# Optimization experiments

Hardware: AMD Instinct MI355X
Metric: run time of the kernel (lower is better)

Reference implementation:

```python
import jax, jax.numpy as jnp
import numpy as np

B, S, H, NH, I = 8, 1024, 1024, 16, 4096
HD = H // NH
EPS = 1e-6
NEG = -1e9


def _glorot(key, shape):
    lim = np.sqrt(6.0 / (shape[0] + shape[1]))
    return jax.random.uniform(key, shape, jnp.float32, -lim, lim)


def setup_inputs() -> dict:
    key = jax.random.key(0)
    ks = jax.random.split(key, 8)
    return {
        "inputs": jax.random.normal(ks[0], (B, S, H), jnp.float32),
        "inputs_mask": jnp.zeros((B, S), jnp.float32),  # 1.0 marks padding
        "attn_qkvw": _glorot(ks[1], (H, 3 * H)),
        "attn_qkvb": jnp.zeros((3 * H,), jnp.float32),
        "attn_ow": _glorot(ks[2], (H, H)),
        "attn_ob": jnp.zeros((H,), jnp.float32),
        "attn_nw": jnp.ones((H,), jnp.float32),
        "attn_nb": jnp.zeros((H,), jnp.float32),
        "inter_w": _glorot(ks[3], (H, I)),
        "inter_b": jnp.zeros((I,), jnp.float32),
        "output_w": _glorot(ks[4], (I, H)),
        "output_b": jnp.zeros((H,), jnp.float32),
        "ffn_nw": jnp.ones((H,), jnp.float32),
        "ffn_nb": jnp.zeros((H,), jnp.float32),
    }


def _layer_norm(x, g, b):
    m = jnp.mean(x, axis=-1, keepdims=True)
    v = jnp.mean(jnp.square(x - m), axis=-1, keepdims=True)
    return (x - m) * jax.lax.rsqrt(v + EPS) * g + b


def reference(inputs, inputs_mask, attn_qkvw, attn_qkvb, attn_ow, attn_ob,
              attn_nw, attn_nb, inter_w, inter_b, output_w, output_b,
              ffn_nw, ffn_nb):
    # ---- self-attention block (pre-LN) ----
    res = inputs
    x = _layer_norm(inputs, attn_nw, attn_nb)
    qkv = x @ attn_qkvw + attn_qkvb                      # [B,S,3H]
    q, k, v = jnp.split(qkv, 3, axis=-1)
    q = q.reshape(B, S, NH, HD)
    k = k.reshape(B, S, NH, HD)
    v = v.reshape(B, S, NH, HD)
    scale = 1.0 / np.sqrt(HD)
    scores = jnp.einsum("bqhd,bkhd->bhqk", q, k) * scale
    scores = scores + inputs_mask[:, None, None, :] * NEG
    probs = jax.nn.softmax(scores, axis=-1)
    ctx = jnp.einsum("bhqk,bkhd->bqhd", probs, v).reshape(B, S, H)
    attn_out = ctx @ attn_ow + attn_ob
    x = res + attn_out
    # ---- FFN block (pre-LN, ReLU) ----
    res2 = x
    y = _layer_norm(x, ffn_nw, ffn_nb)
    h = jax.nn.relu(y @ inter_w + inter_b)
    return res2 + h @ output_w + output_b
```

## Files before the change

kernel.cpp:

```cpp
#include <hip/hip_runtime.h>
#include <cstdint>
#include <cstddef>

typedef _Float16 f16;
typedef _Float16 half8 __attribute__((ext_vector_type(8)));
typedef _Float16 half4v __attribute__((ext_vector_type(4)));
typedef float floatx4 __attribute__((ext_vector_type(4)));
typedef float floatx16 __attribute__((ext_vector_type(16)));

__device__ __forceinline__ floatx4 mfma16(half8 a, half8 b, floatx4 c) {
    return __builtin_amdgcn_mfma_f32_16x16x32_f16(a, b, c, 0, 0, 0);
}
__device__ __forceinline__ floatx16 mfma32(half8 a, half8 b, floatx16 c) {
    return __builtin_amdgcn_mfma_f32_32x32x16_f16(a, b, c, 0, 0, 0);
}

__device__ __forceinline__ void async16(const f16* g, f16* l) {
    __builtin_amdgcn_global_load_lds(
        (const __attribute__((address_space(1))) unsigned int*)(uintptr_t)g,
        (__attribute__((address_space(3))) unsigned int*)(uintptr_t)l,
        16, 0, 0);
}

__global__ __launch_bounds__(256)
void ln_f16_kernel(const float* __restrict__ x, const float* __restrict__ g,
                   const float* __restrict__ be, f16* __restrict__ y)
{
    int row = blockIdx.x, t = threadIdx.x;
    const float* xr = x + (size_t)row * 1024;
    float4 v = *(const float4*)(xr + t * 4);
    float s1 = v.x + v.y + v.z + v.w;
    float s2 = v.x * v.x + v.y * v.y + v.z * v.z + v.w * v.w;
    #pragma unroll
    for (int off = 32; off >= 1; off >>= 1) {
        s1 += __shfl_xor(s1, off);
        s2 += __shfl_xor(s2, off);
    }
    __shared__ float r1[4], r2[4];
    if ((t & 63) == 0) { r1[t >> 6] = s1; r2[t >> 6] = s2; }
    __syncthreads();
    s1 = r1[0] + r1[1] + r1[2] + r1[3];
    s2 = r2[0] + r2[1] + r2[2] + r2[3];
    float mean = s1 * 0.0009765625f;
    float var  = s2 * 0.0009765625f - mean * mean;
    float rs = rsqrtf(var + 1e-6f);
    float4 gv = *(const float4*)(g + t * 4);
    float4 bv = *(const float4*)(be + t * 4);
    half4v o;
    o[0] = (f16)((v.x - mean) * rs * gv.x + bv.x);
    o[1] = (f16)((v.y - mean) * rs * gv.y + bv.y);
    o[2] = (f16)((v.z - mean) * rs * gv.z + bv.z);
    o[3] = (f16)((v.w - mean) * rs * gv.w + bv.w);
    *(half4v*)(y + (size_t)row * 1024 + t * 4) = o;
}

__global__ __launch_bounds__(256)
void transpose_f16_kernel(const float* __restrict__ W, f16* __restrict__ WT,
                          int R, int C)
{
    __shared__ float tile[32][33];
    int tx = threadIdx.x & 31, ty0 = threadIdx.x >> 5;
    int r0 = blockIdx.y * 32, c0 = blockIdx.x * 32;
    #pragma unroll
    for (int i = 0; i < 4; ++i)
        tile[ty0 + i * 8][tx] = W[(size_t)(r0 + ty0 + i * 8) * C + c0 + tx];
    __syncthreads();
    #pragma unroll
    for (int i = 0; i < 4; ++i)
        WT[(size_t)(c0 + ty0 + i * 8) * R + r0 + tx] = (f16)tile[tx][ty0 + i * 8];
}

__global__ __launch_bounds__(256, 2)
void gemm_kernel(const f16* __restrict__ A, const f16* __restrict__ BT,
                 const float* __restrict__ bias, const float* __restrict__ res,
                 float* __restrict__ Cf32, int M, int N, int K)
{
    __shared__ __align__(16) f16 As[2][128 * 64];
    __shared__ __align__(16) f16 Bs[2][128 * 64];
    int m0 = blockIdx.x * 128, n0 = blockIdx.y * 128;
    int t = threadIdx.x, lane = t & 63, wave = t >> 6;
    int quad = lane >> 4, l16 = lane & 15;
    int wm = (wave & 1) * 64, wn = (wave >> 1) * 64;
    int sw = l16 & 7;
    floatx4 acc[4][4] = {};

    const f16* gA[4]; const f16* gB[4]; int oS[4];
    #pragma unroll
    for (int c = 0; c < 4; ++c) {
        int s = c * 256 + t;
        int row = s >> 3, lg = (s & 7) ^ (row & 7);
        gA[c] = A  + (size_t)(m0 + row) * K + lg * 8;
        gB[c] = BT + (size_t)(n0 + row) * K + lg * 8;
        oS[c] = (c * 256 + (t & ~63)) * 8;
    }

    #pragma unroll
    for (int c = 0; c < 4; ++c) {
        async16(gA[c], As[0] + oS[c]);
        async16(gB[c], Bs[0] + oS[c]);
    }
    __syncthreads();

    int buf = 0;
    for (int k0 = 0; k0 < K; k0 += 64) {
        int kn = k0 + 64;
        if (kn < K) {
            #pragma unroll
            for (int c = 0; c < 4; ++c) {
                async16(gA[c] + kn, As[buf ^ 1] + oS[c]);
                async16(gB[c] + kn, Bs[buf ^ 1] + oS[c]);
            }
        }
        #pragma unroll
        for (int ks = 0; ks < 2; ++ks) {
            int ca = (ks * 4 + quad) ^ sw;
            half8 a[4], b[4];
            #pragma unroll
            for (int i = 0; i < 4; ++i) {
                a[i] = *(const half8*)(As[buf] + (wm + i * 16 + l16) * 64 + ca * 8);
                b[i] = *(const half8*)(Bs[buf] + (wn + i * 16 + l16) * 64 + ca * 8);
            }
            #pragma unroll
            for (int i = 0; i < 4; ++i)
                #pragma unroll
                for (int j = 0; j < 4; ++j)
                    acc[i][j] = mfma16(a[i], b[j], acc[i][j]);
        }
        __syncthreads();
        buf ^= 1;
    }

    #pragma unroll
    for (int j = 0; j < 4; ++j) {
        int col = n0 + wn + j * 16 + l16;
        float bv = bias[col];
        #pragma unroll
        for (int i = 0; i < 4; ++i) {
            int rowb = m0 + wm + i * 16 + quad * 4;
            #pragma unroll
            for (int r = 0; r < 4; ++r) {
                float v = acc[i][j][r] + bv;
                size_t idx = (size_t)(rowb + r) * N + col;
                Cf32[idx] = v + res[idx];
            }
        }
    }
}

template<int MODE>
__global__ __launch_bounds__(256, 2)
void gemm_big_kernel(const f16* __restrict__ A, const f16* __restrict__ BT,
                     const float* __restrict__ bias, f16* __restrict__ Cf16,
                     f16* __restrict__ qb, f16* __restrict__ kb, f16* __restrict__ vb,
                     int M, int N, int K)
{
    __shared__ __align__(16) f16 As[256 * 64];
    __shared__ __align__(16) f16 Bs[128 * 64];
    int m0 = blockIdx.x * 256, n0 = blockIdx.y * 128;
    int t = threadIdx.x, lane = t & 63, wave = t >> 6;
    int l32 = lane & 31, kg = lane >> 5;
    int swz = l32 & 7;
    floatx16 acc[2][4];
    #pragma unroll
    for (int mi = 0; mi < 2; ++mi)
        #pragma unroll
        for (int jn = 0; jn < 4; ++jn)
            #pragma unroll
            for (int r = 0; r < 16; ++r) acc[mi][jn][r] = 0.f;

    for (int k0 = 0; k0 < K; k0 += 64) {
        __syncthreads();
        #pragma unroll
        for (int c = 0; c < 8; ++c) {
            int s = c * 256 + t;
            int row = s >> 3, phys = s & 7;
            int lg = phys ^ (row & 7);
            async16(A + (size_t)(m0 + row) * K + k0 + lg * 8,
                    As + (size_t)(c * 256 + (t & ~63)) * 8);
        }
        #pragma unroll
        for (int c = 0; c < 4; ++c) {
            int s = c * 256 + t;
            int row = s >> 3, phys = s & 7;
            int lg = phys ^ (row & 7);
            async16(BT + (size_t)(n0 + row) * K + k0 + lg * 8,
                    Bs + (size_t)(c * 256 + (t & ~63)) * 8);
        }
        __syncthreads();
        #pragma unroll
        for (int ss = 0; ss < 4; ++ss) {
            int ca = (ss * 2 + kg) ^ swz;
            half8 a[2], b[4];
            #pragma unroll
            for (int mi = 0; mi < 2; ++mi)
                a[mi] = *(const half8*)(As + (wave * 64 + mi * 32 + l32) * 64 + ca * 8);
            #pragma unroll
            for (int jn = 0; jn < 4; ++jn)
                b[jn] = *(const half8*)(Bs + (jn * 32 + l32) * 64 + ca * 8);
            #pragma unroll
            for (int mi = 0; mi < 2; ++mi)
                #pragma unroll
                for (int jn = 0; jn < 4; ++jn)
                    acc[mi][jn] = mfma32(a[mi], b[jn], acc[mi][jn]);
        }
    }

    #pragma unroll
    for (int mi = 0; mi < 2; ++mi) {
        int mbase = m0 + wave * 64 + mi * 32 + 4 * kg;
        #pragma unroll
        for (int jn = 0; jn < 4; ++jn) {
            int col = n0 + jn * 32 + l32;
            float bv = bias[col];
            if (MODE == 1) {
                #pragma unroll
                for (int reg = 0; reg < 16; ++reg) {
                    int row = mbase + (reg & 3) + 8 * (reg >> 2);
                    Cf16[(size_t)row * N + col] = (f16)fmaxf(acc[mi][jn][reg] + bv, 0.f);
                }
            } else {
                int part = col >> 10;
                int h = (col >> 6) & 15;
                int d = col & 63;
                if (part == 2) {
                    #pragma unroll
                    for (int rb = 0; rb < 4; ++rb) {
                        int m = mbase + 8 * rb;
                        int bb = m >> 10, s = m & 1023;
                        size_t bh = (size_t)bb * 16 + h;
                        half4v pv;
                        #pragma unroll
                        for (int r = 0; r < 4; ++r) pv[r] = (f16)(acc[mi][jn][rb * 4 + r] + bv);
                        *(half4v*)(vb + (bh * 64 + d) * 1024 + s) = pv;
                    }
                } else {
                    f16* dst0 = part == 0 ? qb : kb;
                    #pragma unroll
                    for (int reg = 0; reg < 16; ++reg) {
                        int m = mbase + (reg & 3) + 8 * (reg >> 2);
                        int bb = m >> 10, s = m & 1023;
                        size_t bh = (size_t)bb * 16 + h;
                        dst0[(bh * 1024 + s) * 64 + d] = (f16)(acc[mi][jn][reg] + bv);
                    }
                }
            }
        }
    }
}

__global__ __launch_bounds__(256)
void attn_kernel(const f16* __restrict__ qb, const f16* __restrict__ kb,
                 const f16* __restrict__ vb, const float* __restrict__ mask,
                 f16* __restrict__ ctx)
{
    const int S = 1024;
    int qt = blockIdx.x, h = blockIdx.y, b = blockIdx.z;
    size_t bh = (size_t)b * 16 + h;
    int t = threadIdx.x, lane = t & 63, wv = t >> 6;
    int quad = lane >> 4, l16 = lane & 15;
    int sw = l16 & 7;

    __shared__ __align__(16) f16 Ks[64 * 64];
    __shared__ __align__(16) f16 Vs[64 * 64];
    __shared__ __align__(16) f16 Ps[4][16 * 40];

    int q0 = qt * 64 + wv * 16;
    const f16* qrow = qb + (bh * 1024 + q0 + l16) * 64;
    half8 aq0 = *(const half8*)(qrow + quad * 8);
    half8 aq1 = *(const half8*)(qrow + 32 + quad * 8);

    floatx4 o[4] = {};
    float lsum[4] = {0.f, 0.f, 0.f, 0.f};
    const float scale = 0.125f;
    const float* mrow = mask + b * S;

    for (int kc = 0; kc < S; kc += 64) {
        __syncthreads();
        #pragma unroll
        for (int c = 0; c < 2; ++c) {
            int s = c * 256 + t;
            int row = s >> 3, phys = s & 7;
            int lg = phys ^ (row & 7);
            f16* lk = Ks + (size_t)(c * 256 + (t & ~63)) * 8;
            f16* lv = Vs + (size_t)(c * 256 + (t & ~63)) * 8;
            async16(kb + (bh * 1024 + kc + row) * 64 + lg * 8, lk);
            async16(vb + (bh * 64 + row) * 1024 + kc + lg * 8, lv);
        }
        __syncthreads();

        floatx4 sf[4];
        #pragma unroll
        for (int cg = 0; cg < 4; ++cg) {
            const f16* kr = Ks + (cg * 16 + l16) * 64;
            int c0 = quad ^ sw;
            half8 b0 = *(const half8*)(kr + c0 * 8);
            half8 b1 = *(const half8*)(kr + (c0 ^ 4) * 8);
            floatx4 z = {};
            sf[cg] = mfma16(aq1, b1, mfma16(aq0, b0, z));
        }
        #pragma unroll
        for (int cg = 0; cg < 4; ++cg) {
            float mk = mrow[kc + cg * 16 + l16] * (-1e9f);
            #pragma unroll
            for (int r = 0; r < 4; ++r) {
                float e = __expf(sf[cg][r] * scale + mk);
                lsum[r] += e;
                Ps[wv][(quad * 4 + r) * 40 + cg * 16 + l16] = (f16)e;
            }
        }
        half8 ap0 = *(const half8*)(Ps[wv] + l16 * 40 + quad * 8);
        half8 ap1 = *(const half8*)(Ps[wv] + l16 * 40 + 32 + quad * 8);
        #pragma unroll
        for (int td = 0; td < 4; ++td) {
            const f16* vr = Vs + (td * 16 + l16) * 64;
            int c0 = quad ^ sw;
            half8 bv0 = *(const half8*)(vr + c0 * 8);
            half8 bv1 = *(const half8*)(vr + (c0 ^ 4) * 8);
            o[td] = mfma16(ap0, bv0, o[td]);
            o[td] = mfma16(ap1, bv1, o[td]);
        }
    }

    #pragma unroll
    for (int r = 0; r < 4; ++r) {
        float s = lsum[r];
        s += __shfl_xor(s, 1); s += __shfl_xor(s, 2);
        s += __shfl_xor(s, 4); s += __shfl_xor(s, 8);
        lsum[r] = 1.f / s;
    }
    #pragma unroll
    for (int td = 0; td < 4; ++td)
        #pragma unroll
        for (int r = 0; r < 4; ++r)
            ctx[((size_t)b * 1024 + q0 + quad * 4 + r) * 1024 + h * 64 + td * 16 + l16]
                = (f16)(o[td][r] * lsum[r]);
}

extern "C" void kernel_launch(void* const* d_in, const int* in_sizes, int n_in,
                              void* d_out, int out_size, void* d_ws, size_t ws_size,
                              hipStream_t stream)
{
    const float* inputs = (const float*)d_in[0];
    const float* mask   = (const float*)d_in[1];
    const float* qkvw   = (const float*)d_in[2];
    const float* qkvb   = (const float*)d_in[3];
    const float* ow     = (const float*)d_in[4];
    const float* ob     = (const float*)d_in[5];
    const float* anw    = (const float*)d_in[6];
    const float* anb    = (const float*)d_in[7];
    const float* iw     = (const float*)d_in[8];
    const float* ib     = (const float*)d_in[9];
    const float* outw   = (const float*)d_in[10];
    const float* outb   = (const float*)d_in[11];
    const float* fnw    = (const float*)d_in[12];
    const float* fnb    = (const float*)d_in[13];
    float* out = (float*)d_out;

    const int M = 8192;
    uint8_t* ws = (uint8_t*)d_ws;
    f16* wT_qkv = (f16*)(ws + 0);
    f16* wT_o   = (f16*)(ws + 6291456);
    f16* wT_i   = (f16*)(ws + 8388608);
    f16* wT_out = (f16*)(ws + 16777216);
    f16* xln    = (f16*)(ws + 25165824);
    float* x1   = (float*)(ws + 41943040);
    f16* qbuf   = (f16*)(ws + 75497472);
    f16* kbuf   = (f16*)(ws + 92274688);
    f16* vbuf   = (f16*)(ws + 109051904);
    f16* ctx    = (f16*)(ws + 125829120);
    f16* hbuf   = (f16*)(ws + 75497472);

    transpose_f16_kernel<<<dim3(96, 32),  256, 0, stream>>>(qkvw, wT_qkv, 1024, 3072);
    transpose_f16_kernel<<<dim3(32, 32),  256, 0, stream>>>(ow,   wT_o,   1024, 1024);
    transpose_f16_kernel<<<dim3(128, 32), 256, 0, stream>>>(iw,   wT_i,   1024, 4096);
    transpose_f16_kernel<<<dim3(32, 128), 256, 0, stream>>>(outw, wT_out, 4096, 1024);

    ln_f16_kernel<<<8192, 256, 0, stream>>>(inputs, anw, anb, xln);

    gemm_big_kernel<2><<<dim3(32, 24), 256, 0, stream>>>(xln, wT_qkv, qkvb,
        nullptr, qbuf, kbuf, vbuf, M, 3072, 1024);

    attn_kernel<<<dim3(16, 16, 8), 256, 0, stream>>>(qbuf, kbuf, vbuf, mask, ctx);

    gemm_kernel<<<dim3(64, 8), 256, 0, stream>>>(ctx, wT_o, ob, inputs,
        x1, M, 1024, 1024);

    ln_f16_kernel<<<8192, 256, 0, stream>>>(x1, fnw, fnb, xln);

    gemm_big_kernel<1><<<dim3(32, 32), 256, 0, stream>>>(xln, wT_i, ib,
        hbuf, nullptr, nullptr, nullptr, M, 4096, 1024);

    gemm_kernel<<<dim3(64, 8), 256, 0, stream>>>(hbuf, wT_out, outb, x1,
        out, M, 1024, 4096);
}
```

Measured before the change: 469.4 us.

## Double-buffer LDS tiles in big GEMM to overlap global loads with MFMA

The big GEMM kernel now keeps two LDS buffers for the A and B tiles and issues async global-to-LDS loads for the next K-step before computing on the current one. One barrier per iteration replaces two, and global pointers and LDS offsets are precomputed once outside the loop. LDS use doubles to 96KB per block, so launch bounds drop to one block per CU and occupancy falls. The reduced latency hiding from fewer resident blocks may offset the overlap.

```diff
diff --git a/kernel.cpp b/kernel.cpp
--- a/kernel.cpp
+++ b/kernel.cpp
@@ -148,14 +148,14 @@
 }
 
 template<int MODE>
-__global__ __launch_bounds__(256, 2)
+__global__ __launch_bounds__(256, 1)
 void gemm_big_kernel(const f16* __restrict__ A, const f16* __restrict__ BT,
                      const float* __restrict__ bias, f16* __restrict__ Cf16,
                      f16* __restrict__ qb, f16* __restrict__ kb, f16* __restrict__ vb,
                      int M, int N, int K)
 {
-    __shared__ __align__(16) f16 As[256 * 64];
-    __shared__ __align__(16) f16 Bs[128 * 64];
+    __shared__ __align__(16) f16 As[2][256 * 64];
+    __shared__ __align__(16) f16 Bs[2][128 * 64];
     int m0 = blockIdx.x * 256, n0 = blockIdx.y * 128;
     int t = threadIdx.x, lane = t & 63, wave = t >> 6;
     int l32 = lane & 31, kg = lane >> 5;
@@ -168,41 +168,56 @@
             #pragma unroll
             for (int r = 0; r < 16; ++r) acc[mi][jn][r] = 0.f;
 
+    const f16* gA[8]; int oA[8];
+    #pragma unroll
+    for (int c = 0; c < 8; ++c) {
+        int s = c * 256 + t;
+        int row = s >> 3, lg = (s & 7) ^ (row & 7);
+        gA[c] = A + (size_t)(m0 + row) * K + lg * 8;
+        oA[c] = (c * 256 + (t & ~63)) * 8;
+    }
+    const f16* gB[4]; int oB[4];
+    #pragma unroll
+    for (int c = 0; c < 4; ++c) {
+        int s = c * 256 + t;
+        int row = s >> 3, lg = (s & 7) ^ (row & 7);
+        gB[c] = BT + (size_t)(n0 + row) * K + lg * 8;
+        oB[c] = (c * 256 + (t & ~63)) * 8;
+    }
+
+    #pragma unroll
+    for (int c = 0; c < 8; ++c) async16(gA[c], As[0] + oA[c]);
+    #pragma unroll
+    for (int c = 0; c < 4; ++c) async16(gB[c], Bs[0] + oB[c]);
+    __syncthreads();
+
+    int buf = 0;
     for (int k0 = 0; k0 < K; k0 += 64) {
-        __syncthreads();
-        #pragma unroll
-        for (int c = 0; c < 8; ++c) {
-            int s = c * 256 + t;
-            int row = s >> 3, phys = s & 7;
-            int lg = phys ^ (row & 7);
-            async16(A + (size_t)(m0 + row) * K + k0 + lg * 8,
-                    As + (size_t)(c * 256 + (t & ~63)) * 8);
-        }
-        #pragma unroll
-        for (int c = 0; c < 4; ++c) {
-            int s = c * 256 + t;
-            int row = s >> 3, phys = s & 7;
-            int lg = phys ^ (row & 7);
-            async16(BT + (size_t)(n0 + row) * K + k0 + lg * 8,
-                    Bs + (size_t)(c * 256 + (t & ~63)) * 8);
-        }
-        __syncthreads();
+        int kn = k0 + 64;
+        if (kn < K) {
+            #pragma unroll
+            for (int c = 0; c < 8; ++c) async16(gA[c] + kn, As[buf ^ 1] + oA[c]);
+            #pragma unroll
+            for (int c = 0; c < 4; ++c) async16(gB[c] + kn, Bs[buf ^ 1] + oB[c]);
+        }
         #pragma unroll
         for (int ss = 0; ss < 4; ++ss) {
             int ca = (ss * 2 + kg) ^ swz;
             half8 a[2], b[4];
             #pragma unroll
             for (int mi = 0; mi < 2; ++mi)
-                a[mi] = *(const half8*)(As + (wave * 64 + mi * 32 + l32) * 64 + ca * 8);
+                a[mi] = *(const half8*)(As[buf] + (wave * 64 + mi * 32 + l32) * 64 + ca * 8);
             #pragma unroll
             for (int jn = 0; jn < 4; ++jn)
-                b[jn] = *(const half8*)(Bs + (jn * 32 + l32) * 64 + ca * 8);
+                b[jn] = *(const half8*)(Bs[buf] + (jn * 32 + l32) * 64 + ca * 8);
             #pragma unroll
             for (int mi = 0; mi < 2; ++mi)
                 #pragma unroll
                 for (int jn = 0; jn < 4; ++jn)
                     acc[mi][jn] = mfma32(a[mi], b[jn], acc[mi][jn]);
         }
+        __syncthreads();
+        buf ^= 1;
     }
 
     #pragma unroll
```

Measured after the change: 476.3 us. No clear change (+1.5%).
